# Optimization experiments

Hardware: AMD Instinct MI355X
Metric: run time of the kernel (lower is better)

The kernel has to match this reference:

```python
import jax, jax.numpy as jnp
import numpy as np

B, N, NE = 64, 512, 500
FIELD_DIM, E_DIM, HIDDEN, LATENT = 256, 64, 512, 256


def _lin_init(key, fan_in, fan_out):
    kw, kb = jax.random.split(key)
    s = 1.0 / np.sqrt(fan_in)
    W = jax.random.uniform(kw, (fan_in, fan_out), minval=-s, maxval=s, dtype=jnp.float32)
    b = jax.random.uniform(kb, (fan_out,), minval=-s, maxval=s, dtype=jnp.float32)
    return W, b


def setup_inputs() -> dict:
    key = jax.random.key(0)
    ks = jax.random.split(key, 16)
    inp = {}
    inp['field_atom_lat'] = jax.random.normal(ks[0], (B, N, FIELD_DIM), dtype=jnp.float32)
    inp['mask'] = jax.random.randint(ks[1], (B, N), 0, 2).astype(bool)
    inp['e_feat'] = jax.random.normal(ks[2], (NE, E_DIM), dtype=jnp.float32)
    # query MLP (3 layers): e_dim -> hidden -> hidden -> latent
    inp['q_w1'], inp['q_b1'] = _lin_init(ks[3], E_DIM, HIDDEN)
    inp['q_w2'], inp['q_b2'] = _lin_init(ks[4], HIDDEN, HIDDEN)
    inp['q_w3'], inp['q_b3'] = _lin_init(ks[5], HIDDEN, LATENT)
    # key MLP (3 layers): field_dim -> hidden -> hidden -> latent
    inp['k_w1'], inp['k_b1'] = _lin_init(ks[6], FIELD_DIM, HIDDEN)
    inp['k_w2'], inp['k_b2'] = _lin_init(ks[7], HIDDEN, HIDDEN)
    inp['k_w3'], inp['k_b3'] = _lin_init(ks[8], HIDDEN, LATENT)
    # value MLP (3 layers)
    inp['v_w1'], inp['v_b1'] = _lin_init(ks[9], FIELD_DIM, HIDDEN)
    inp['v_w2'], inp['v_b2'] = _lin_init(ks[10], HIDDEN, HIDDEN)
    inp['v_w3'], inp['v_b3'] = _lin_init(ks[11], HIDDEN, LATENT)
    # out MLP (2 layers): latent -> hidden -> latent
    inp['o_w1'], inp['o_b1'] = _lin_init(ks[12], LATENT, HIDDEN)
    inp['o_w2'], inp['o_b2'] = _lin_init(ks[13], HIDDEN, LATENT)
    return inp


def _mlp3(x, w1, b1, w2, b2, w3, b3):
    h = jax.nn.silu(x @ w1 + b1)
    h = jax.nn.silu(h @ w2 + b2)
    return h @ w3 + b3


def _mlp2(x, w1, b1, w2, b2):
    return jax.nn.silu(x @ w1 + b1) @ w2 + b2


def reference(field_atom_lat, mask, e_feat,
              q_w1, q_b1, q_w2, q_b2, q_w3, q_b3,
              k_w1, k_b1, k_w2, k_b2, k_w3, k_b3,
              v_w1, v_b1, v_w2, v_b2, v_w3, v_b3,
              o_w1, o_b1, o_w2, o_b2):
    latent_dim = q_w3.shape[1]
    scale = latent_dim ** (-0.5)
    q = _mlp3(e_feat, q_w1, q_b1, q_w2, q_b2, q_w3, q_b3)          # [nE, L] (shared across batch)
    k = _mlp3(field_atom_lat, k_w1, k_b1, k_w2, k_b2, k_w3, k_b3)  # [B, N, L]
    v = _mlp3(field_atom_lat, v_w1, v_b1, v_w2, v_b2, v_w3, v_b3)  # [B, N, L]
    scores = jnp.einsum('el,bnl->ben', q, k) * scale               # [B, nE, N]
    scores = jnp.where(mask[:, None, :], scores, jnp.float32(-1e9))
    attn = jax.nn.softmax(scores, axis=2)
    attn = attn * mask[:, None, :].astype(attn.dtype)              # post-softmax mask, as in torch
    out = jnp.einsum('ben,bnl->bel', attn, v)                      # [B, nE, L]
    return _mlp2(out, o_w1, o_b1, o_w2, o_b2)
```

## Files before the change

kernel.cpp:

```cpp
#include <hip/hip_runtime.h>
#include <math.h>

#define BATCH 64
#define N_ATOMS 512
#define NE 500
#define FIELD_DIM 256
#define E_DIM 64
#define HIDDEN 512
#define LATENT 256

typedef short bf16x8 __attribute__((ext_vector_type(8)));
typedef unsigned short u16x8 __attribute__((ext_vector_type(8)));
typedef unsigned short u16x4 __attribute__((ext_vector_type(4)));
typedef float f32x4 __attribute__((ext_vector_type(4)));

__device__ __forceinline__ unsigned short f2bf(float x) {
    unsigned u = __float_as_uint(x);
    unsigned r = (u + 0x7FFFu + ((u >> 16) & 1u)) >> 16;
    return (unsigned short)r;
}
__device__ __forceinline__ float bf2f(unsigned short b) {
    return __uint_as_float(((unsigned)b) << 16);
}
__device__ __forceinline__ float silu_f(float x) { return x / (1.f + __expf(-x)); }

#define GLOAD_LDS16(gptr, lptr)                                                   \
    __builtin_amdgcn_global_load_lds(                                             \
        (const __attribute__((address_space(1))) void*)(gptr),                    \
        (__attribute__((address_space(3))) void*)(lptr), 16, 0, 0)

#define QW1 0
#define QW2 32768
#define QW3 294912
#define KW1 425984
#define KW2 557056
#define KW3 819200
#define VW1 950272
#define VW2 1081344
#define VW3 1343488
#define OW1 1474560
#define OW2 1605632

template <int K, bool SILU>
__device__ __forceinline__ void mlp_layer_ip(
    const unsigned short* __restrict__ Wg, const float* __restrict__ Bg,
    unsigned short* buf, int wave, int lane, int fr, int fq)
{
    constexpr int NS = K / 32;
    const int fb = wave * 64;
    const unsigned short* wp = Wg + (long long)(wave * 4) * NS * 512 + lane * 8;

    f32x4 acc[4][4];
#pragma unroll
    for (int mf = 0; mf < 4; mf++)
#pragma unroll
        for (int nf = 0; nf < 4; nf++) acc[mf][nf] = (f32x4)0.f;

    bf16x8 wfA[4], wfB[4];
#pragma unroll
    for (int mf = 0; mf < 4; mf++)
        wfA[mf] = *reinterpret_cast<const bf16x8*>(wp + (long long)mf * NS * 512);
#pragma unroll
    for (int mf = 0; mf < 4; mf++)
        wfB[mf] = *reinterpret_cast<const bf16x8*>(wp + ((long long)mf * NS + 1) * 512);

#pragma unroll
    for (int ks = 0; ks < NS; ks++) {
        bf16x8 wfC[4];
        if (ks + 2 < NS) {
#pragma unroll
            for (int mf = 0; mf < 4; mf++)
                wfC[mf] = *reinterpret_cast<const bf16x8*>(
                    wp + ((long long)mf * NS + (ks + 2)) * 512);
        }
        bf16x8 bfr[4];
#pragma unroll
        for (int nf = 0; nf < 4; nf++) {
            int row = nf * 16 + fr;
            bfr[nf] = *reinterpret_cast<const bf16x8*>(
                (const char*)buf + row * (K * 2) +
                ((ks * 64 + fq * 16) ^ ((row & 7) << 4)));
        }
        __builtin_amdgcn_s_setprio(1);
#pragma unroll
        for (int mf = 0; mf < 4; mf++)
#pragma unroll
            for (int nf = 0; nf < 4; nf++)
                acc[mf][nf] = __builtin_amdgcn_mfma_f32_16x16x32_bf16(
                    wfA[mf], bfr[nf], acc[mf][nf], 0, 0, 0);
        __builtin_amdgcn_s_setprio(0);
#pragma unroll
        for (int mf = 0; mf < 4; mf++) wfA[mf] = wfB[mf];
        if (ks + 2 < NS) {
#pragma unroll
            for (int mf = 0; mf < 4; mf++) wfB[mf] = wfC[mf];
        }
    }
    __syncthreads();

#pragma unroll
    for (int mf = 0; mf < 4; mf++) {
        f32x4 bv = *reinterpret_cast<const f32x4*>(Bg + fb + mf * 16 + fq * 4);
#pragma unroll
        for (int nf = 0; nf < 4; nf++) {
            int row = nf * 16 + fr;
            u16x4 ov;
#pragma unroll
            for (int r = 0; r < 4; r++) {
                float x = acc[mf][nf][r] + bv[r];
                if (SILU) x = silu_f(x);
                ov[r] = f2bf(x);
            }
            *reinterpret_cast<u16x4*>(
                (char*)buf + row * 1024 +
                ((fb * 2 + mf * 32 + fq * 8) ^ ((row & 7) << 4))) = ov;
        }
    }
    __syncthreads();
}

template <int K, bool SILU>
__device__ __forceinline__ void mlp_layer_io(
    const unsigned short* __restrict__ Wg, const float* __restrict__ Bg,
    const unsigned short* inb, unsigned short* outb, int wave, int lane,
    int fr, int fq)
{
    constexpr int NS = K / 32;
    const int fb = wave * 64;
    const unsigned short* wp = Wg + (long long)(wave * 4) * NS * 512 + lane * 8;

    f32x4 acc[4][4];
#pragma unroll
    for (int mf = 0; mf < 4; mf++)
#pragma unroll
        for (int nf = 0; nf < 4; nf++) acc[mf][nf] = (f32x4)0.f;

    bf16x8 wfA[4], wfB[4];
#pragma unroll
    for (int mf = 0; mf < 4; mf++)
        wfA[mf] = *reinterpret_cast<const bf16x8*>(wp + (long long)mf * NS * 512);
#pragma unroll
    for (int mf = 0; mf < 4; mf++)
        wfB[mf] = *reinterpret_cast<const bf16x8*>(wp + ((long long)mf * NS + 1) * 512);

#pragma unroll
    for (int ks = 0; ks < NS; ks++) {
        bf16x8 wfC[4];
        if (ks + 2 < NS) {
#pragma unroll
            for (int mf = 0; mf < 4; mf++)
                wfC[mf] = *reinterpret_cast<const bf16x8*>(
                    wp + ((long long)mf * NS + (ks + 2)) * 512);
        }
        bf16x8 bfr[4];
#pragma unroll
        for (int nf = 0; nf < 4; nf++) {
            int row = nf * 16 + fr;
            bfr[nf] = *reinterpret_cast<const bf16x8*>(
                (const char*)inb + row * (K * 2) +
                ((ks * 64 + fq * 16) ^ ((row & 7) << 4)));
        }
        __builtin_amdgcn_s_setprio(1);
#pragma unroll
        for (int mf = 0; mf < 4; mf++)
#pragma unroll
            for (int nf = 0; nf < 4; nf++)
                acc[mf][nf] = __builtin_amdgcn_mfma_f32_16x16x32_bf16(
                    wfA[mf], bfr[nf], acc[mf][nf], 0, 0, 0);
        __builtin_amdgcn_s_setprio(0);
#pragma unroll
        for (int mf = 0; mf < 4; mf++) wfA[mf] = wfB[mf];
        if (ks + 2 < NS) {
#pragma unroll
            for (int mf = 0; mf < 4; mf++) wfB[mf] = wfC[mf];
        }
    }

#pragma unroll
    for (int mf = 0; mf < 4; mf++) {
        f32x4 bv = *reinterpret_cast<const f32x4*>(Bg + fb + mf * 16 + fq * 4);
#pragma unroll
        for (int nf = 0; nf < 4; nf++) {
            int row = nf * 16 + fr;
            u16x4 ov;
#pragma unroll
            for (int r = 0; r < 4; r++) {
                float x = acc[mf][nf][r] + bv[r];
                if (SILU) x = silu_f(x);
                ov[r] = f2bf(x);
            }
            *reinterpret_cast<u16x4*>(
                (char*)outb + row * 1024 +
                ((fb * 2 + mf * 32 + fq * 8) ^ ((row & 7) << 4))) = ov;
        }
    }
    __syncthreads();
}

__device__ __forceinline__ void mlp_final512(
    const unsigned short* __restrict__ Wg, const float* __restrict__ Bg,
    const unsigned short* buf, int wave, int lane, int fr, int fq,
    f32x4 (&acc)[2][4])
{
    const int fb = wave * 32;
    const unsigned short* wp = Wg + (long long)(wave * 2) * 16 * 512 + lane * 8;
#pragma unroll
    for (int mf = 0; mf < 2; mf++)
#pragma unroll
        for (int nf = 0; nf < 4; nf++) acc[mf][nf] = (f32x4)0.f;

    bf16x8 wfA[2], wfB[2];
#pragma unroll
    for (int mf = 0; mf < 2; mf++)
        wfA[mf] = *reinterpret_cast<const bf16x8*>(wp + (long long)mf * 16 * 512);
#pragma unroll
    for (int mf = 0; mf < 2; mf++)
        wfB[mf] = *reinterpret_cast<const bf16x8*>(wp + ((long long)mf * 16 + 1) * 512);

#pragma unroll
    for (int ks = 0; ks < 16; ks++) {
        bf16x8 wfC[2];
        if (ks + 2 < 16) {
#pragma unroll
            for (int mf = 0; mf < 2; mf++)
                wfC[mf] = *reinterpret_cast<const bf16x8*>(
                    wp + ((long long)mf * 16 + (ks + 2)) * 512);
        }
        bf16x8 bfr[4];
#pragma unroll
        for (int nf = 0; nf < 4; nf++) {
            int row = nf * 16 + fr;
            bfr[nf] = *reinterpret_cast<const bf16x8*>(
                (const char*)buf + row * 1024 +
                ((ks * 64 + fq * 16) ^ ((row & 7) << 4)));
        }
        __builtin_amdgcn_s_setprio(1);
#pragma unroll
        for (int mf = 0; mf < 2; mf++)
#pragma unroll
            for (int nf = 0; nf < 4; nf++)
                acc[mf][nf] = __builtin_amdgcn_mfma_f32_16x16x32_bf16(
                    wfA[mf], bfr[nf], acc[mf][nf], 0, 0, 0);
        __builtin_amdgcn_s_setprio(0);
#pragma unroll
        for (int mf = 0; mf < 2; mf++) wfA[mf] = wfB[mf];
        if (ks + 2 < 16) {
#pragma unroll
            for (int mf = 0; mf < 2; mf++) wfB[mf] = wfC[mf];
        }
    }
#pragma unroll
    for (int mf = 0; mf < 2; mf++) {
        f32x4 bv = *reinterpret_cast<const f32x4*>(Bg + fb + mf * 16 + fq * 4);
#pragma unroll
        for (int nf = 0; nf < 4; nf++)
#pragma unroll
            for (int r = 0; r < 4; r++) acc[mf][nf][r] += bv[r];
    }
}

__global__ __launch_bounds__(512, 2) void fused_qkv(
    const unsigned short* __restrict__ field_bf,
    const unsigned short* __restrict__ efeat_bf,
    const unsigned short* __restrict__ wt,
    const float* __restrict__ qb1, const float* __restrict__ qb2,
    const float* __restrict__ qb3, const float* __restrict__ kb1,
    const float* __restrict__ kb2, const float* __restrict__ kb3,
    const float* __restrict__ vb1, const float* __restrict__ vb2,
    const float* __restrict__ vb3,
    unsigned short* __restrict__ qbuf,
    unsigned short* __restrict__ kbuf,
    unsigned short* __restrict__ vtb)
{
    __shared__ unsigned short buf[64 * 512];
    const int t = threadIdx.x, wave = t >> 6, lane = t & 63;
    const int fr = lane & 15, fq = lane >> 4;
    const int bid = blockIdx.x;

    if (bid < 1024) {
        const int isv = bid >> 9;
        const int m0  = (bid & 511) * 64;
        const unsigned short* W1 = wt + (isv ? VW1 : KW1);
        const unsigned short* W2 = wt + (isv ? VW2 : KW2);
        const unsigned short* W3 = wt + (isv ? VW3 : KW3);
        const float* B1 = isv ? vb1 : kb1;
        const float* B2 = isv ? vb2 : kb2;
        const float* B3 = isv ? vb3 : kb3;

#pragma unroll
        for (int c = wave; c < 32; c += 8) {
            int gi  = c * 64 + lane;
            int row = gi >> 5;
            int g   = gi & 31;
            int gs  = (g & ~7) | ((g & 7) ^ (row & 7));
            GLOAD_LDS16(field_bf + (long long)(m0 + row) * 256 + gs * 8, buf + c * 512);
        }
        __syncthreads();

        mlp_layer_ip<256, true>(W1, B1, buf, wave, lane, fr, fq);
        mlp_layer_ip<512, true>(W2, B2, buf, wave, lane, fr, fq);
        f32x4 acc[2][4];
        mlp_final512(W3, B3, buf, wave, lane, fr, fq, acc);

        if (!isv) {
#pragma unroll
            for (int mf = 0; mf < 2; mf++)
#pragma unroll
                for (int nf = 0; nf < 4; nf++) {
                    int row = m0 + nf * 16 + fr;
                    u16x4 ov;
#pragma unroll
                    for (int r = 0; r < 4; r++) ov[r] = f2bf(acc[mf][nf][r]);
                    *reinterpret_cast<u16x4*>(
                        kbuf + (long long)row * 256 + wave * 32 + mf * 16 + fq * 4) = ov;
                }
        } else {
            __syncthreads();
#pragma unroll
            for (int mf = 0; mf < 2; mf++)
#pragma unroll
                for (int nf = 0; nf < 4; nf++) {
                    int row = nf * 16 + fr;
                    u16x4 ov;
#pragma unroll
                    for (int r = 0; r < 4; r++) ov[r] = f2bf(acc[mf][nf][r]);
                    *reinterpret_cast<u16x4*>(
                        (char*)buf + row * 512 +
                        ((wave * 64 + mf * 32 + fq * 8) ^ ((row & 7) << 4))) = ov;
                }
            __syncthreads();
            int l  = t >> 1;
            int nh = (t & 1) * 32;
            int b  = m0 >> 9, nb = m0 & 511;
            long long base = ((long long)b * 256 + l) * 512 + nb + nh;
#pragma unroll
            for (int q = 0; q < 4; q++) {
                u16x8 ov;
#pragma unroll
                for (int j = 0; j < 8; j++) {
                    int n = nh + q * 8 + j;
                    ov[j] = *reinterpret_cast<const unsigned short*>(
                        (const char*)buf + n * 512 + ((l * 2) ^ ((n & 7) << 4)));
                }
                *reinterpret_cast<u16x8*>(vtb + base + q * 8) = ov;
            }
        }
    } else {
        const int m0 = (bid - 1024) * 64;
        {
            int row = t >> 3;
            int g   = lane & 7;
            int gr  = m0 + row; if (gr >= NE) gr = NE - 1;
            int gs  = g ^ (row & 7);
            GLOAD_LDS16(efeat_bf + (long long)gr * 64 + gs * 8, buf + wave * 512);
        }
        __syncthreads();

        mlp_layer_ip<64, true>(wt + QW1, qb1, buf, wave, lane, fr, fq);
        mlp_layer_ip<512, true>(wt + QW2, qb2, buf, wave, lane, fr, fq);
        f32x4 acc[2][4];
        mlp_final512(wt + QW3, qb3, buf, wave, lane, fr, fq, acc);
#pragma unroll
        for (int mf = 0; mf < 2; mf++)
#pragma unroll
            for (int nf = 0; nf < 4; nf++) {
                int row = m0 + nf * 16 + fr;
                if (row < NE) {
                    u16x4 ov;
#pragma unroll
                    for (int r = 0; r < 4; r++) ov[r] = f2bf(acc[mf][nf][r]);
                    *reinterpret_cast<u16x4*>(
                        qbuf + (long long)row * 256 + wave * 32 + mf * 16 + fq * 4) = ov;
                }
            }
    }
}

__global__ __launch_bounds__(512, 1) void attn_fused(
    const unsigned short* __restrict__ qbuf,
    const unsigned short* __restrict__ kbuf,
    const unsigned short* __restrict__ vt,
    const int* __restrict__ mask,
    const unsigned short* __restrict__ wt,
    const float* __restrict__ ob1, const float* __restrict__ ob2,
    float* __restrict__ out)
{
    __shared__ unsigned char LDS[100352];
    unsigned short* Qs = (unsigned short*)LDS;
    unsigned short* Ks = (unsigned short*)(LDS + 32768);
    unsigned short* Ps = (unsigned short*)LDS;
    unsigned short* Vs = (unsigned short*)(LDS + 65536);
    float*          red = (float*)(LDS + 98304);
    unsigned short* oin  = (unsigned short*)(LDS + 65536);
    unsigned short* obuf = (unsigned short*)LDS;

    const int id = blockIdx.x;
    const int b  = id & 63;
    const int e0 = (id >> 6) * 64;
    const int t = threadIdx.x, wave = t >> 6;
    const int lane = t & 63, fr = lane & 15, fq = lane >> 4;
    const int tr = t >> 3, tg = t & 7;

#pragma unroll
    for (int i = 0; i < 4; i++) {
        int ge = e0 + tr; if (ge >= NE) ge = NE - 1;
        int gi = tg ^ (tr & 7);
        GLOAD_LDS16(qbuf + (long long)ge * 256 + i * 64 + gi * 8,
                    Qs + i * 4096 + wave * 512);
    }
#pragma unroll
    for (int j = 0; j < 8; j++) {
        int n  = j * 64 + tr;
        int gi = tg ^ (n & 7);
        GLOAD_LDS16(kbuf + (long long)(b * 512 + n) * 256 + gi * 8,
                    Ks + j * 4096 + wave * 512);
    }
    int mk[4];
#pragma unroll
    for (int nf = 0; nf < 4; nf++) mk[nf] = mask[b * 512 + wave * 64 + nf * 16 + fr];

    f32x4 acc[4][4];
#pragma unroll
    for (int i = 0; i < 4; i++)
#pragma unroll
        for (int j = 0; j < 4; j++) acc[i][j] = (f32x4)0.f;

    __syncthreads();

    for (int ks = 0; ks < 4; ks++) {
#pragma unroll
        for (int h = 0; h < 2; h++) {
            bf16x8 af[4], bv[4];
#pragma unroll
            for (int mf = 0; mf < 4; mf++) {
                int e = mf * 16 + fr;
                int byo = ks * 8192 + e * 128 + ((h * 64 + fq * 16) ^ ((e & 7) << 4));
                af[mf] = *(const bf16x8*)((const char*)Qs + byo);
            }
#pragma unroll
            for (int nf = 0; nf < 4; nf++) {
                int n = wave * 64 + nf * 16 + fr;
                int byo = n * 128 + ((h * 64 + fq * 16) ^ ((n & 7) << 4));
                bv[nf] = *(const bf16x8*)((const char*)Ks + byo);
            }
#pragma unroll
            for (int mf = 0; mf < 4; mf++)
#pragma unroll
                for (int nf = 0; nf < 4; nf++)
                    acc[mf][nf] = __builtin_amdgcn_mfma_f32_16x16x32_bf16(
                        af[mf], bv[nf], acc[mf][nf], 0, 0, 0);
        }
        if (ks < 3) {
            __syncthreads();
#pragma unroll
            for (int j = 0; j < 8; j++) {
                int n  = j * 64 + tr;
                int gi = tg ^ (n & 7);
                GLOAD_LDS16(kbuf + (long long)(b * 512 + n) * 256 + (ks + 1) * 64 + gi * 8,
                            Ks + j * 4096 + wave * 512);
            }
            __syncthreads();
        }
    }

    const float scale = 0.0625f;
#pragma unroll
    for (int mf = 0; mf < 4; mf++)
#pragma unroll
        for (int nf = 0; nf < 4; nf++)
#pragma unroll
            for (int r = 0; r < 4; r++)
                acc[mf][nf][r] = mk[nf] ? acc[mf][nf][r] * scale : -1e9f;

    float gm[4][4];
#pragma unroll
    for (int mf = 0; mf < 4; mf++)
#pragma unroll
        for (int r = 0; r < 4; r++) {
            float m = fmaxf(fmaxf(acc[mf][0][r], acc[mf][1][r]),
                            fmaxf(acc[mf][2][r], acc[mf][3][r]));
#pragma unroll
            for (int off = 1; off < 16; off <<= 1) m = fmaxf(m, __shfl_xor(m, off, 64));
            if (fr == 0) red[(mf * 16 + fq * 4 + r) * 8 + wave] = m;
        }
    __syncthreads();
#pragma unroll
    for (int mf = 0; mf < 4; mf++)
#pragma unroll
        for (int r = 0; r < 4; r++) {
            int row = mf * 16 + fq * 4 + r;
            float4 a = *(float4*)&red[row * 8];
            float4 c = *(float4*)&red[row * 8 + 4];
            gm[mf][r] = fmaxf(fmaxf(fmaxf(a.x, a.y), fmaxf(a.z, a.w)),
                              fmaxf(fmaxf(c.x, c.y), fmaxf(c.z, c.w)));
        }
    __syncthreads();

    float inv[4][4];
#pragma unroll
    for (int mf = 0; mf < 4; mf++)
#pragma unroll
        for (int r = 0; r < 4; r++) {
            float s = 0.f;
#pragma unroll
            for (int nf = 0; nf < 4; nf++) {
                acc[mf][nf][r] = __expf(acc[mf][nf][r] - gm[mf][r]);
                s += acc[mf][nf][r];
            }
#pragma unroll
            for (int off = 1; off < 16; off <<= 1) s += __shfl_xor(s, off, 64);
            if (fr == 0) red[(mf * 16 + fq * 4 + r) * 8 + wave] = s;
        }
    __syncthreads();
#pragma unroll
    for (int mf = 0; mf < 4; mf++)
#pragma unroll
        for (int r = 0; r < 4; r++) {
            int row = mf * 16 + fq * 4 + r;
            float4 a = *(float4*)&red[row * 8];
            float4 c = *(float4*)&red[row * 8 + 4];
            inv[mf][r] = 1.f / (a.x + a.y + a.z + a.w + c.x + c.y + c.z + c.w);
        }

#pragma unroll
    for (int mf = 0; mf < 4; mf++)
#pragma unroll
        for (int nf = 0; nf < 4; nf++)
#pragma unroll
            for (int r = 0; r < 4; r++) {
                int row = mf * 16 + fq * 4 + r;
                int c   = wave * 64 + nf * 16 + fr;
                float pv = mk[nf] ? acc[mf][nf][r] * inv[mf][r] : 0.f;
                *(unsigned short*)((char*)Ps + row * 1024 + ((c * 2) ^ ((row & 7) << 4))) =
                    f2bf(pv);
            }
    __syncthreads();

    f32x4 acc2[4][2];
#pragma unroll
    for (int i = 0; i < 4; i++)
#pragma unroll
        for (int j = 0; j < 2; j++) acc2[i][j] = (f32x4)0.f;

#pragma unroll
    for (int j = 0; j < 4; j++) {
        int l  = j * 64 + tr;
        int gi = tg ^ (l & 7);
        GLOAD_LDS16(vt + (long long)(b * 256 + l) * 512 + gi * 8,
                    Vs + j * 4096 + wave * 512);
    }
    __syncthreads();

    for (int ks = 0; ks < 8; ks++) {
#pragma unroll
        for (int h = 0; h < 2; h++) {
            bf16x8 af[4], bv[2];
#pragma unroll
            for (int mf = 0; mf < 4; mf++) {
                int e = mf * 16 + fr;
                int byo = e * 1024 + ((ks * 128 + h * 64 + fq * 16) ^ ((e & 7) << 4));
                af[mf] = *(const bf16x8*)((const char*)Ps + byo);
            }
#pragma unroll
            for (int nf = 0; nf < 2; nf++) {
                int l = wave * 32 + nf * 16 + fr;
                int byo = l * 128 + ((h * 64 + fq * 16) ^ ((l & 7) << 4));
                bv[nf] = *(const bf16x8*)((const char*)Vs + byo);
            }
#pragma unroll
            for (int mf = 0; mf < 4; mf++)
#pragma unroll
                for (int nf = 0; nf < 2; nf++)
                    acc2[mf][nf] = __builtin_amdgcn_mfma_f32_16x16x32_bf16(
                        af[mf], bv[nf], acc2[mf][nf], 0, 0, 0);
        }
        if (ks < 7) {
            __syncthreads();
#pragma unroll
            for (int j = 0; j < 4; j++) {
                int l  = j * 64 + tr;
                int gi = tg ^ (l & 7);
                GLOAD_LDS16(vt + (long long)(b * 256 + l) * 512 + (ks + 1) * 64 + gi * 8,
                            Vs + j * 4096 + wave * 512);
            }
            __syncthreads();
        }
    }

    __syncthreads();
#pragma unroll
    for (int mf = 0; mf < 4; mf++)
#pragma unroll
        for (int nf = 0; nf < 2; nf++)
#pragma unroll
            for (int r = 0; r < 4; r++) {
                int row = mf * 16 + fq * 4 + r;
                int col = wave * 32 + nf * 16 + fr;
                *(unsigned short*)((char*)oin + row * 512 +
                                   ((col * 2) ^ ((row & 7) << 4))) =
                    f2bf(acc2[mf][nf][r]);
            }
    __syncthreads();

    mlp_layer_io<256, true>(wt + OW1, ob1, oin, obuf, wave, lane, fr, fq);
    f32x4 oacc[2][4];
    mlp_final512(wt + OW2, ob2, obuf, wave, lane, fr, fq, oacc);

#pragma unroll
    for (int mf = 0; mf < 2; mf++)
#pragma unroll
        for (int nf = 0; nf < 4; nf++) {
            int e = e0 + nf * 16 + fr;
            if (e < NE)
                *reinterpret_cast<f32x4*>(
                    out + ((long long)b * NE + e) * 256 + wave * 32 + mf * 16 + fq * 4) =
                    oacc[mf][nf];
        }
}

__global__ __launch_bounds__(256) void f32_to_bf16(
    const float* __restrict__ in, unsigned short* __restrict__ out, long long n8)
{
    long long i      = (long long)blockIdx.x * 256 + threadIdx.x;
    long long stride = (long long)gridDim.x * 256;
    for (; i < n8; i += stride) {
        const float4* p = reinterpret_cast<const float4*>(in + i * 8);
        float4 a = p[0], b = p[1];
        u16x8 o;
        o[0] = f2bf(a.x); o[1] = f2bf(a.y); o[2] = f2bf(a.z); o[3] = f2bf(a.w);
        o[4] = f2bf(b.x); o[5] = f2bf(b.y); o[6] = f2bf(b.z); o[7] = f2bf(b.w);
        *reinterpret_cast<u16x8*>(out + i * 8) = o;
    }
}

__global__ __launch_bounds__(256) void wt_pack(
    const float* w0, const float* w1, const float* w2, const float* w3,
    const float* w4, const float* w5, const float* w6, const float* w7,
    const float* w8, const float* w9, const float* w10, unsigned short* dst)
{
    const int Kd[11] = {64, 512, 512, 256, 512, 512, 256, 512, 512, 256, 512};
    const int Nd[11] = {512, 512, 256, 512, 512, 256, 512, 512, 256, 512, 256};
    const long long Od[11] = {QW1, QW2, QW3, KW1, KW2, KW3, VW1, VW2, VW3, OW1, OW2};
    const int z = blockIdx.z;
    const float* src = z == 0 ? w0 : z == 1 ? w1 : z == 2 ? w2 : z == 3 ? w3 :
                       z == 4 ? w4 : z == 5 ? w5 : z == 6 ? w6 : z == 7 ? w7 :
                       z == 8 ? w8 : z == 9 ? w9 : w10;
    const int K = Kd[z], N = Nd[z];
    const int k0 = blockIdx.y * 64, n0 = blockIdx.x * 64;
    if (k0 >= K || n0 >= N) return;

    __shared__ float tf[64][65];
    const int t = threadIdx.x;
    {
        const int r = t >> 2;
        const int c0 = (t & 3) * 16;
        const float* srow = src + (long long)(k0 + r) * N + n0 + c0;
#pragma unroll
        for (int q = 0; q < 4; q++) {
            float4 xv = *reinterpret_cast<const float4*>(srow + q * 4);
            tf[r][c0 + q * 4 + 0] = xv.x;
            tf[r][c0 + q * 4 + 1] = xv.y;
            tf[r][c0 + q * 4 + 2] = xv.z;
            tf[r][c0 + q * 4 + 3] = xv.w;
        }
    }
    __syncthreads();

#pragma unroll
    for (int it = 0; it < 2; it++) {
        int wi = t + it * 256;
        int nc = wi & 63;
        int k8 = wi >> 6;
        int kg = k0 + k8 * 8;
        int ks = kg >> 5;
        int fq = (kg >> 3) & 3;
        int f16 = (n0 + nc) >> 4;
        int fr  = nc & 15;
        u16x8 ov;
#pragma unroll
        for (int e = 0; e < 8; e++) ov[e] = f2bf(tf[k8 * 8 + e][nc]);
        long long off = Od[z] +
            (((long long)f16 * (K / 32) + ks) * 64 + fq * 16 + fr) * 8;
        *reinterpret_cast<u16x8*>(dst + off) = ov;
    }
}

extern "C" void kernel_launch(void* const* d_in, const int* in_sizes, int n_in,
                              void* d_out, int out_size, void* d_ws, size_t ws_size,
                              hipStream_t stream)
{
    const float* field = (const float*)d_in[0];
    const int*   mask  = (const int*)d_in[1];
    const float* efeat = (const float*)d_in[2];
    const float* q_w1 = (const float*)d_in[3];  const float* q_b1 = (const float*)d_in[4];
    const float* q_w2 = (const float*)d_in[5];  const float* q_b2 = (const float*)d_in[6];
    const float* q_w3 = (const float*)d_in[7];  const float* q_b3 = (const float*)d_in[8];
    const float* k_w1 = (const float*)d_in[9];  const float* k_b1 = (const float*)d_in[10];
    const float* k_w2 = (const float*)d_in[11]; const float* k_b2 = (const float*)d_in[12];
    const float* k_w3 = (const float*)d_in[13]; const float* k_b3 = (const float*)d_in[14];
    const float* v_w1 = (const float*)d_in[15]; const float* v_b1 = (const float*)d_in[16];
    const float* v_w2 = (const float*)d_in[17]; const float* v_b2 = (const float*)d_in[18];
    const float* v_w3 = (const float*)d_in[19]; const float* v_b3 = (const float*)d_in[20];
    const float* o_w1 = (const float*)d_in[21]; const float* o_b1 = (const float*)d_in[22];
    const float* o_w2 = (const float*)d_in[23]; const float* o_b2 = (const float*)d_in[24];

    unsigned short* ws = (unsigned short*)d_ws;
    unsigned short* field_bf = ws;
    unsigned short* efeat_bf = ws + 8388608;
    unsigned short* wt       = ws + 8420608;
    unsigned short* qbuf     = ws + 10157312;
    unsigned short* kbuf     = ws + 10285312;
    unsigned short* vtb      = ws + 18673920;

    f32_to_bf16<<<dim3(2048), dim3(256), 0, stream>>>(field, field_bf, 1048576);
    f32_to_bf16<<<dim3(16),   dim3(256), 0, stream>>>(efeat, efeat_bf, 4000);
    wt_pack<<<dim3(8, 8, 11), dim3(256), 0, stream>>>(
        q_w1, q_w2, q_w3, k_w1, k_w2, k_w3, v_w1, v_w2, v_w3, o_w1, o_w2, wt);

    fused_qkv<<<dim3(1032), dim3(512), 0, stream>>>(
        field_bf, efeat_bf, wt, q_b1, q_b2, q_b3, k_b1, k_b2, k_b3,
        v_b1, v_b2, v_b3, qbuf, kbuf, vtb);

    attn_fused<<<dim3(512), dim3(512), 0, stream>>>(
        qbuf, kbuf, vtb, mask, wt, o_b1, o_b2, (float*)d_out);
}
```

Measured before the change: 210.3 us.

## Stage MLP weight fragments through double-buffered LDS via async global-to-LDS loads

The QKV MLP layers stop loading weight fragments into registers with a two-step register prefetch. They now stream each k-step's weights into a double-buffered LDS staging area using global_load_lds, with a block barrier every k-step. This is meant to cut register pressure and hide global latency through async copies. The extra 64KB of shared memory drops occupancy to one block per CU (launch bounds changed to 512,1), and the per-step __syncthreads adds synchronization overhead.

```diff
diff --git a/kernel.cpp b/kernel.cpp
--- a/kernel.cpp
+++ b/kernel.cpp
@@ -41,14 +41,15 @@
 #define OW1 1474560
 #define OW2 1605632
 
+#define WSLOT 16384
+
 template <int K, bool SILU>
-__device__ __forceinline__ void mlp_layer_ip(
+__device__ __forceinline__ void mlp_layer_ls(
     const unsigned short* __restrict__ Wg, const float* __restrict__ Bg,
-    unsigned short* buf, int wave, int lane, int fr, int fq)
+    unsigned short* buf, unsigned short* Wst, int wave, int lane, int fr, int fq)
 {
     constexpr int NS = K / 32;
     const int fb = wave * 64;
-    const unsigned short* wp = Wg + (long long)(wave * 4) * NS * 512 + lane * 8;
 
     f32x4 acc[4][4];
 #pragma unroll
@@ -56,23 +57,27 @@
 #pragma unroll
         for (int nf = 0; nf < 4; nf++) acc[mf][nf] = (f32x4)0.f;
 
-    bf16x8 wfA[4], wfB[4];
-#pragma unroll
-    for (int mf = 0; mf < 4; mf++)
-        wfA[mf] = *reinterpret_cast<const bf16x8*>(wp + (long long)mf * NS * 512);
-#pragma unroll
-    for (int mf = 0; mf < 4; mf++)
-        wfB[mf] = *reinterpret_cast<const bf16x8*>(wp + ((long long)mf * NS + 1) * 512);
+#pragma unroll
+    for (int mf = 0; mf < 4; mf++)
+        GLOAD_LDS16(Wg + (((long long)(wave * 4 + mf)) * NS + 0) * 512 + lane * 8,
+                    Wst + (wave * 4 + mf) * 512);
+    __syncthreads();
 
 #pragma unroll
     for (int ks = 0; ks < NS; ks++) {
-        bf16x8 wfC[4];
-        if (ks + 2 < NS) {
+        const int p = ks & 1;
+        if (ks + 1 < NS) {
 #pragma unroll
             for (int mf = 0; mf < 4; mf++)
-                wfC[mf] = *reinterpret_cast<const bf16x8*>(
-                    wp + ((long long)mf * NS + (ks + 2)) * 512);
-        }
+                GLOAD_LDS16(
+                    Wg + (((long long)(wave * 4 + mf)) * NS + (ks + 1)) * 512 + lane * 8,
+                    Wst + (p ^ 1) * WSLOT + (wave * 4 + mf) * 512);
+        }
+        bf16x8 wf[4];
+#pragma unroll
+        for (int mf = 0; mf < 4; mf++)
+            wf[mf] = *reinterpret_cast<const bf16x8*>(
+                Wst + p * WSLOT + (wave * 4 + mf) * 512 + lane * 8);
         bf16x8 bfr[4];
 #pragma unroll
         for (int nf = 0; nf < 4; nf++) {
@@ -87,16 +92,10 @@
 #pragma unroll
             for (int nf = 0; nf < 4; nf++)
                 acc[mf][nf] = __builtin_amdgcn_mfma_f32_16x16x32_bf16(
-                    wfA[mf], bfr[nf], acc[mf][nf], 0, 0, 0);
+                    wf[mf], bfr[nf], acc[mf][nf], 0, 0, 0);
         __builtin_amdgcn_s_setprio(0);
-#pragma unroll
-        for (int mf = 0; mf < 4; mf++) wfA[mf] = wfB[mf];
-        if (ks + 2 < NS) {
-#pragma unroll
-            for (int mf = 0; mf < 4; mf++) wfB[mf] = wfC[mf];
-        }
-    }
-    __syncthreads();
+        __syncthreads();
+    }
 
 #pragma unroll
     for (int mf = 0; mf < 4; mf++) {
@@ -117,6 +116,66 @@
         }
     }
     __syncthreads();
+}
+
+__device__ __forceinline__ void mlp_final_ls(
+    const unsigned short* __restrict__ Wg, const float* __restrict__ Bg,
+    const unsigned short* buf, unsigned short* Wst, int wave, int lane,
+    int fr, int fq, f32x4 (&acc)[2][4])
+{
+    const int fb = wave * 32;
+#pragma unroll
+    for (int mf = 0; mf < 2; mf++)
+#pragma unroll
+        for (int nf = 0; nf < 4; nf++) acc[mf][nf] = (f32x4)0.f;
+
+#pragma unroll
+    for (int mf = 0; mf < 2; mf++)
+        GLOAD_LDS16(Wg + (((long long)(wave * 2 + mf)) * 16 + 0) * 512 + lane * 8,
+                    Wst + (wave * 2 + mf) * 512);
+    __syncthreads();
+
+#pragma unroll
+    for (int ks = 0; ks < 16; ks++) {
+        const int p = ks & 1;
+        if (ks + 1 < 16) {
+#pragma unroll
+            for (int mf = 0; mf < 2; mf++)
+                GLOAD_LDS16(
+                    Wg + (((long long)(wave * 2 + mf)) * 16 + (ks + 1)) * 512 + lane * 8,
+                    Wst + (p ^ 1) * WSLOT + (wave * 2 + mf) * 512);
+        }
+        bf16x8 wf[2];
+#pragma unroll
+        for (int mf = 0; mf < 2; mf++)
+            wf[mf] = *reinterpret_cast<const bf16x8*>(
+                Wst + p * WSLOT + (wave * 2 + mf) * 512 + lane * 8);
+        bf16x8 bfr[4];
+#pragma unroll
+        for (int nf = 0; nf < 4; nf++) {
+            int row = nf * 16 + fr;
+            bfr[nf] = *reinterpret_cast<const bf16x8*>(
+                (const char*)buf + row * 1024 +
+                ((ks * 64 + fq * 16) ^ ((row & 7) << 4)));
+        }
+        __builtin_amdgcn_s_setprio(1);
+#pragma unroll
+        for (int mf = 0; mf < 2; mf++)
+#pragma unroll
+            for (int nf = 0; nf < 4; nf++)
+                acc[mf][nf] = __builtin_amdgcn_mfma_f32_16x16x32_bf16(
+                    wf[mf], bfr[nf], acc[mf][nf], 0, 0, 0);
+        __builtin_amdgcn_s_setprio(0);
+        __syncthreads();
+    }
+#pragma unroll
+    for (int mf = 0; mf < 2; mf++) {
+        f32x4 bv = *reinterpret_cast<const f32x4*>(Bg + fb + mf * 16 + fq * 4);
+#pragma unroll
+        for (int nf = 0; nf < 4; nf++)
+#pragma unroll
+            for (int r = 0; r < 4; r++) acc[mf][nf][r] += bv[r];
+    }
 }
 
 template <int K, bool SILU>
@@ -259,7 +318,7 @@
     }
 }
 
-__global__ __launch_bounds__(512, 2) void fused_qkv(
+__global__ __launch_bounds__(512, 1) void fused_qkv(
     const unsigned short* __restrict__ field_bf,
     const unsigned short* __restrict__ efeat_bf,
     const unsigned short* __restrict__ wt,
@@ -273,6 +332,7 @@
     unsigned short* __restrict__ vtb)
 {
     __shared__ unsigned short buf[64 * 512];
+    __shared__ unsigned short Wst[2 * WSLOT];
     const int t = threadIdx.x, wave = t >> 6, lane = t & 63;
     const int fr = lane & 15, fq = lane >> 4;
     const int bid = blockIdx.x;
@@ -297,10 +357,10 @@
         }
         __syncthreads();
 
-        mlp_layer_ip<256, true>(W1, B1, buf, wave, lane, fr, fq);
-        mlp_layer_ip<512, true>(W2, B2, buf, wave, lane, fr, fq);
+        mlp_layer_ls<256, true>(W1, B1, buf, Wst, wave, lane, fr, fq);
+        mlp_layer_ls<512, true>(W2, B2, buf, Wst, wave, lane, fr, fq);
         f32x4 acc[2][4];
-        mlp_final512(W3, B3, buf, wave, lane, fr, fq, acc);
+        mlp_final_ls(W3, B3, buf, Wst, wave, lane, fr, fq, acc);
 
         if (!isv) {
 #pragma unroll
@@ -356,10 +416,10 @@
         }
         __syncthreads();
 
-        mlp_layer_ip<64, true>(wt + QW1, qb1, buf, wave, lane, fr, fq);
-        mlp_layer_ip<512, true>(wt + QW2, qb2, buf, wave, lane, fr, fq);
+        mlp_layer_ls<64, true>(wt + QW1, qb1, buf, Wst, wave, lane, fr, fq);
+        mlp_layer_ls<512, true>(wt + QW2, qb2, buf, Wst, wave, lane, fr, fq);
         f32x4 acc[2][4];
-        mlp_final512(wt + QW3, qb3, buf, wave, lane, fr, fq, acc);
+        mlp_final_ls(wt + QW3, qb3, buf, Wst, wave, lane, fr, fq, acc);
 #pragma unroll
         for (int mf = 0; mf < 2; mf++)
 #pragma unroll
```

Result: slower. 252.5 us (+20.0%).
